# Optimization experiments

Measured on AMD Instinct MI355X. Metric: run time of the kernel, lower is better.

Reference implementation:

```python
import jax, jax.numpy as jnp
import numpy as np

OUT, IN = 4096, 4096
BITS = 4
B, S = 4, 2048


def setup_inputs() -> dict:
    key = jax.random.key(0)
    k1, k2, k3, k4, k5, k6 = jax.random.split(key, 6)
    x = jax.random.normal(k1, (B, S, IN), dtype=jnp.float32)
    indices = jax.random.randint(k2, (OUT, IN), 0, 2 ** BITS, dtype=jnp.int32)
    centroids = jax.random.normal(k3, (2 ** BITS,), dtype=jnp.float32)
    # Pi stands in for the seeded rotation matrix (orthogonality not required for math check)
    Pi = jax.random.normal(k4, (IN, IN), dtype=jnp.float32) / np.sqrt(IN)
    row_norms = jax.random.uniform(k5, (OUT,), dtype=jnp.float32) + 0.5
    bias = jax.random.normal(k6, (OUT,), dtype=jnp.float32)
    return {"x": x, "indices": indices, "centroids": centroids, "Pi": Pi,
            "row_norms": row_norms, "bias": bias}


def reference(x, indices, centroids, Pi, row_norms, bias):
    # Dequantize: centroid gather -> inverse rotation -> per-row rescale
    y_hat = centroids[indices]                    # (out, in)
    W = (y_hat @ Pi) * row_norms[:, None]         # (out, in)
    # F.linear: x @ W^T + b
    return jnp.einsum('bsi,oi->bso', x, W) + bias
```

## Files before the change

### kernel.cpp

```cpp
#include <hip/hip_runtime.h>
#include <hip/hip_bf16.h>

typedef unsigned short u16;
typedef __bf16 bf16x8 __attribute__((ext_vector_type(8)));
typedef float f32x16 __attribute__((ext_vector_type(16)));


__device__ __forceinline__ u16 f32_to_bf16(float f) {
    unsigned int u = __float_as_uint(f);
    unsigned int r = (u + 0x7FFFu + ((u >> 16) & 1u)) >> 16;
    return (u16)r;
}

__device__ __forceinline__ unsigned pack2(float a, float b) {
    return (unsigned)f32_to_bf16(a) | ((unsigned)f32_to_bf16(b) << 16);
}

__device__ __forceinline__ void load_lds16(const void* g, void* s) {
    __builtin_amdgcn_global_load_lds(
        (__attribute__((address_space(1))) void*)g,
        (__attribute__((address_space(3))) void*)s,
        16, 0, 0);
}


__global__ __launch_bounds__(256) void convert_f32_bf16(
        const float* __restrict__ in, u16* __restrict__ out) {
    int i = blockIdx.x * 256 + threadIdx.x;
    const float4* in4 = (const float4*)in;
    float4 v0 = in4[(size_t)i * 2];
    float4 v1 = in4[(size_t)i * 2 + 1];
    uint4 r;
    r.x = pack2(v0.x, v0.y);
    r.y = pack2(v0.z, v0.w);
    r.z = pack2(v1.x, v1.y);
    r.w = pack2(v1.z, v1.w);
    ((uint4*)out)[i] = r;
}


__global__ __launch_bounds__(256) void dequant_kernel(
        const int* __restrict__ idx, const float* __restrict__ cent,
        u16* __restrict__ out) {
    __shared__ float lut[16];
    if (threadIdx.x < 16) lut[threadIdx.x] = cent[threadIdx.x];
    __syncthreads();
    int i = blockIdx.x * 256 + threadIdx.x;
    const int4* in4 = (const int4*)idx;
    int4 a = in4[(size_t)i * 2];
    int4 b = in4[(size_t)i * 2 + 1];
    uint4 r;
    r.x = pack2(lut[a.x], lut[a.y]);
    r.y = pack2(lut[a.z], lut[a.w]);
    r.z = pack2(lut[b.x], lut[b.y]);
    r.w = pack2(lut[b.z], lut[b.w]);
    ((uint4*)out)[i] = r;
}


__global__ __launch_bounds__(256) void transpose_to_bf16(
        const float* __restrict__ Pi, u16* __restrict__ PiT) {
    __shared__ float tile[32][33];
    const int tx = threadIdx.x;
    const int ty = threadIdx.y;
    const int j0 = blockIdx.x * 32;
    const int k0 = blockIdx.y * 32;
#pragma unroll
    for (int i = 0; i < 4; i++)
        tile[ty + 8 * i][tx] = Pi[(size_t)(k0 + ty + 8 * i) * 4096 + j0 + tx];
    __syncthreads();
#pragma unroll
    for (int i = 0; i < 4; i++)
        PiT[(size_t)(j0 + ty + 8 * i) * 4096 + k0 + tx] =
            f32_to_bf16(tile[tx][ty + 8 * i]);
}


template <int MODE>
__global__ __launch_bounds__(256) void gemm_bt(
        const u16* __restrict__ A, const u16* __restrict__ Bm,
        const float* __restrict__ aux, float* __restrict__ Cf,
        u16* __restrict__ Cb, int M, int N, int K) {
    __shared__ u16 As[2 * 128 * 32];
    __shared__ u16 Bs[2 * 128 * 32];

    const int tid  = threadIdx.x;
    const int lane = tid & 63;
    const int wv   = tid >> 6;
    const int wr   = (wv >> 1) << 6;
    const int wc   = (wv & 1) << 6;
    const int m0   = blockIdx.y * 128;
    const int n0   = blockIdx.x * 128;

    const int rT  = tid >> 2;
    const int cSw = (((tid & 3) ^ ((rT >> 1) & 3)) << 3);
    const u16* Ag = A + (size_t)(m0 + rT) * K + cSw;
    const u16* Bg = Bm + (size_t)(n0 + rT) * K + cSw;
    u16* Asd = &As[tid * 8];
    u16* Bsd = &Bs[tid * 8];

    const int mrow = lane & 31;
    const int kc   = lane >> 5;
    int offA[2][2], offB[2][2];
#pragma unroll
    for (int mi = 0; mi < 2; mi++) {
        const int r  = wr + mi * 32 + mrow;
        const int sw = (r >> 1) & 3;
#pragma unroll
        for (int s = 0; s < 2; s++)
            offA[mi][s] = r * 32 + (((s * 2 + kc) ^ sw) << 3);
    }
#pragma unroll
    for (int ni = 0; ni < 2; ni++) {
        const int r  = wc + ni * 32 + mrow;
        const int sw = (r >> 1) & 3;
#pragma unroll
        for (int s = 0; s < 2; s++)
            offB[ni][s] = r * 32 + (((s * 2 + kc) ^ sw) << 3);
    }

    f32x16 acc[2][2];
#pragma unroll
    for (int i = 0; i < 2; i++)
#pragma unroll
        for (int j = 0; j < 2; j++)
#pragma unroll
            for (int e = 0; e < 16; e++) acc[i][j][e] = 0.f;

    for (int k0 = 0; k0 < K; k0 += 64) {
        load_lds16(Ag + k0, Asd);
        load_lds16(Ag + (size_t)64 * K + k0, Asd + 64 * 32);
        load_lds16(Bg + k0, Bsd);
        load_lds16(Bg + (size_t)64 * K + k0, Bsd + 64 * 32);
        load_lds16(Ag + k0 + 32, Asd + 4096);
        load_lds16(Ag + (size_t)64 * K + k0 + 32, Asd + 4096 + 64 * 32);
        load_lds16(Bg + k0 + 32, Bsd + 4096);
        load_lds16(Bg + (size_t)64 * K + k0 + 32, Bsd + 4096 + 64 * 32);
        __syncthreads();

#pragma unroll
        for (int h = 0; h < 2; h++) {
            const int hb = h * 4096;
            bf16x8 af[2][2], bfv[2][2];
#pragma unroll
            for (int mi = 0; mi < 2; mi++)
#pragma unroll
                for (int s = 0; s < 2; s++)
                    af[mi][s] = *(const bf16x8*)&As[hb + offA[mi][s]];
#pragma unroll
            for (int ni = 0; ni < 2; ni++)
#pragma unroll
                for (int s = 0; s < 2; s++)
                    bfv[ni][s] = *(const bf16x8*)&Bs[hb + offB[ni][s]];
#pragma unroll
            for (int s = 0; s < 2; s++)
#pragma unroll
                for (int mi = 0; mi < 2; mi++)
#pragma unroll
                    for (int ni = 0; ni < 2; ni++)
                        acc[mi][ni] = __builtin_amdgcn_mfma_f32_32x32x16_bf16(
                            af[mi][s], bfv[ni][s], acc[mi][ni], 0, 0, 0);
        }
        __syncthreads();
    }

    const int colf = lane & 31;
    const int r4   = (lane >> 5) << 2;
#pragma unroll
    for (int mi = 0; mi < 2; mi++) {
#pragma unroll
        for (int ni = 0; ni < 2; ni++) {
            const int col = n0 + wc + ni * 32 + colf;
            float bv = 0.f;
            if (MODE == 1) bv = aux[col];
#pragma unroll
            for (int reg = 0; reg < 16; reg++) {
                const int row = m0 + wr + mi * 32 + (reg & 3) + ((reg >> 2) << 3) + r4;
                if (MODE == 0)
                    Cb[(size_t)row * N + col] = f32_to_bf16(acc[mi][ni][reg] * aux[row]);
                else
                    Cf[(size_t)row * N + col] = acc[mi][ni][reg] + bv;
            }
        }
    }
}


extern "C" void kernel_launch(void* const* d_in, const int* in_sizes, int n_in,
                              void* d_out, int out_size, void* d_ws, size_t ws_size,
                              hipStream_t stream) {
    const float* x         = (const float*)d_in[0];
    const int*   indices   = (const int*)d_in[1];
    const float* centroids = (const float*)d_in[2];
    const float* Pi        = (const float*)d_in[3];
    const float* row_norms = (const float*)d_in[4];
    const float* bias      = (const float*)d_in[5];
    float* out = (float*)d_out;

    u16* x_bf = (u16*)d_ws;
    u16* y_bf = x_bf + (size_t)33554432;
    u16* pi_t = y_bf + (size_t)16777216;
    u16* w_bf = pi_t + (size_t)16777216;

    convert_f32_bf16<<<16384, 256, 0, stream>>>(x, x_bf);
    dequant_kernel<<<8192, 256, 0, stream>>>(indices, centroids, y_bf);
    transpose_to_bf16<<<dim3(128, 128), dim3(32, 8), 0, stream>>>(Pi, pi_t);
    gemm_bt<0><<<dim3(32, 32), 256, 0, stream>>>(
        y_bf, pi_t, row_norms, nullptr, w_bf, 4096, 4096, 4096);
    gemm_bt<1><<<dim3(32, 64), 256, 0, stream>>>(
        x_bf, w_bf, bias, out, nullptr, 8192, 4096, 4096);
}
```

Measured before the change: 774.1 us.

## Rewrite GEMM as 256x256-tile, 8-wave kernel with 4-stage LDS pipeline

Replaces the 128x128 double-buffered GEMM with a 256x256 tile computed by 512 threads (8 waves, each 128x64) using 16x16x32 MFMAs. A four-slot LDS ring is filled with direct global-to-LDS loads, and explicit vmcnt waits and barriers let loads overlap compute in half-step phases. It also remaps block IDs in groups of eight for L2 locality and raises wave priority around MFMA bursts. The larger tile cuts global traffic per FLOP but uses 128 KB of LDS and many accumulator registers, which limits occupancy and makes correctness depend on hand-tuned wait counts.

```diff
diff --git a/kernel.cpp b/kernel.cpp
--- a/kernel.cpp
+++ b/kernel.cpp
@@ -3,7 +3,7 @@
 
 typedef unsigned short u16;
 typedef __bf16 bf16x8 __attribute__((ext_vector_type(8)));
-typedef float f32x16 __attribute__((ext_vector_type(16)));
+typedef float f32x4 __attribute__((ext_vector_type(4)));
 
 
 __device__ __forceinline__ u16 f32_to_bf16(float f) {
@@ -77,109 +77,142 @@
 
 
 template <int MODE>
-__global__ __launch_bounds__(256) void gemm_bt(
+__global__ __launch_bounds__(512, 2) void gemm_bt(
         const u16* __restrict__ A, const u16* __restrict__ Bm,
         const float* __restrict__ aux, float* __restrict__ Cf,
         u16* __restrict__ Cb, int M, int N, int K) {
-    __shared__ u16 As[2 * 128 * 32];
-    __shared__ u16 Bs[2 * 128 * 32];
+    __shared__ u16 As[4 * 8192];
+    __shared__ u16 Bs[4 * 8192];
 
     const int tid  = threadIdx.x;
     const int lane = tid & 63;
     const int wv   = tid >> 6;
-    const int wr   = (wv >> 1) << 6;
-    const int wc   = (wv & 1) << 6;
-    const int m0   = blockIdx.y * 128;
-    const int n0   = blockIdx.x * 128;
-
-    const int rT  = tid >> 2;
-    const int cSw = (((tid & 3) ^ ((rT >> 1) & 3)) << 3);
-    const u16* Ag = A + (size_t)(m0 + rT) * K + cSw;
-    const u16* Bg = Bm + (size_t)(n0 + rT) * K + cSw;
-    u16* Asd = &As[tid * 8];
-    u16* Bsd = &Bs[tid * 8];
-
-    const int mrow = lane & 31;
-    const int kc   = lane >> 5;
-    int offA[2][2], offB[2][2];
-#pragma unroll
-    for (int mi = 0; mi < 2; mi++) {
-        const int r  = wr + mi * 32 + mrow;
-        const int sw = (r >> 1) & 3;
-#pragma unroll
-        for (int s = 0; s < 2; s++)
-            offA[mi][s] = r * 32 + (((s * 2 + kc) ^ sw) << 3);
-    }
-#pragma unroll
-    for (int ni = 0; ni < 2; ni++) {
-        const int r  = wc + ni * 32 + mrow;
-        const int sw = (r >> 1) & 3;
-#pragma unroll
-        for (int s = 0; s < 2; s++)
-            offB[ni][s] = r * 32 + (((s * 2 + kc) ^ sw) << 3);
-    }
-
-    f32x16 acc[2][2];
-#pragma unroll
-    for (int i = 0; i < 2; i++)
-#pragma unroll
-        for (int j = 0; j < 2; j++)
-#pragma unroll
-            for (int e = 0; e < 16; e++) acc[i][j][e] = 0.f;
-
-    for (int k0 = 0; k0 < K; k0 += 64) {
-        load_lds16(Ag + k0, Asd);
-        load_lds16(Ag + (size_t)64 * K + k0, Asd + 64 * 32);
-        load_lds16(Bg + k0, Bsd);
-        load_lds16(Bg + (size_t)64 * K + k0, Bsd + 64 * 32);
-        load_lds16(Ag + k0 + 32, Asd + 4096);
-        load_lds16(Ag + (size_t)64 * K + k0 + 32, Asd + 4096 + 64 * 32);
-        load_lds16(Bg + k0 + 32, Bsd + 4096);
-        load_lds16(Bg + (size_t)64 * K + k0 + 32, Bsd + 4096 + 64 * 32);
-        __syncthreads();
-
-#pragma unroll
-        for (int h = 0; h < 2; h++) {
-            const int hb = h * 4096;
-            bf16x8 af[2][2], bfv[2][2];
-#pragma unroll
-            for (int mi = 0; mi < 2; mi++)
-#pragma unroll
-                for (int s = 0; s < 2; s++)
-                    af[mi][s] = *(const bf16x8*)&As[hb + offA[mi][s]];
-#pragma unroll
-            for (int ni = 0; ni < 2; ni++)
-#pragma unroll
-                for (int s = 0; s < 2; s++)
-                    bfv[ni][s] = *(const bf16x8*)&Bs[hb + offB[ni][s]];
-#pragma unroll
-            for (int s = 0; s < 2; s++)
-#pragma unroll
-                for (int mi = 0; mi < 2; mi++)
-#pragma unroll
-                    for (int ni = 0; ni < 2; ni++)
-                        acc[mi][ni] = __builtin_amdgcn_mfma_f32_32x32x16_bf16(
-                            af[mi][s], bfv[ni][s], acc[mi][ni], 0, 0, 0);
-        }
-        __syncthreads();
-    }
-
-    const int colf = lane & 31;
-    const int r4   = (lane >> 5) << 2;
-#pragma unroll
-    for (int mi = 0; mi < 2; mi++) {
-#pragma unroll
-        for (int ni = 0; ni < 2; ni++) {
-            const int col = n0 + wc + ni * 32 + colf;
-            float bv = 0.f;
-            if (MODE == 1) bv = aux[col];
-#pragma unroll
-            for (int reg = 0; reg < 16; reg++) {
-                const int row = m0 + wr + mi * 32 + (reg & 3) + ((reg >> 2) << 3) + r4;
-                if (MODE == 0)
-                    Cb[(size_t)row * N + col] = f32_to_bf16(acc[mi][ni][reg] * aux[row]);
-                else
-                    Cf[(size_t)row * N + col] = acc[mi][ni][reg] + bv;
+    const int wr   = wv >> 2;
+    const int wc   = wv & 3;
+
+    const int nwg  = gridDim.x * gridDim.y;
+    const int orig = blockIdx.y * gridDim.x + blockIdx.x;
+    const int swz  = (orig & 7) * (nwg >> 3) + (orig >> 3);
+    const int m0   = (swz >> 4) << 8;
+    const int n0   = (swz & 15) << 8;
+
+    const int sr  = tid >> 2;
+    const int csw = ((tid & 3) ^ ((tid >> 3) & 3)) << 3;
+    const u16* a0 = A  + (size_t)(m0 + sr) * K + csw;
+    const u16* a1 = A  + (size_t)(m0 + 128 + sr) * K + csw;
+    const u16* b0 = Bm + (size_t)(n0 + sr) * K + csw;
+    const u16* b1 = Bm + (size_t)(n0 + 128 + sr) * K + csw;
+    u16* dA = As + tid * 8;
+    u16* dB = Bs + tid * 8;
+
+    const int l15   = lane & 15;
+    const int ck    = (((lane >> 4) ^ ((lane >> 1) & 3)) << 3);
+    const int laneA = (wr * 128 + l15) * 32 + ck;
+    const int laneB = (wc * 64 + l15) * 32 + ck;
+
+    f32x4 acc[8][4];
+#pragma unroll
+    for (int i = 0; i < 8; i++)
+#pragma unroll
+        for (int j = 0; j < 4; j++) acc[i][j] = (f32x4){0.f, 0.f, 0.f, 0.f};
+    bf16x8 bF[4];
+
+#define STAGE_A(SLOT, COL) do { \
+        load_lds16(a0 + (COL), dA + (SLOT) * 8192); \
+        load_lds16(a1 + (COL), dA + (SLOT) * 8192 + 4096); } while (0)
+#define STAGE_B(SLOT, COL) do { \
+        load_lds16(b0 + (COL), dB + (SLOT) * 8192); \
+        load_lds16(b1 + (COL), dB + (SLOT) * 8192 + 4096); } while (0)
+#define VM(N) asm volatile("s_waitcnt vmcnt(" #N ")" ::: "memory")
+
+#define PHASE(SB, MH, RB, STAGE, WAIT) do { \
+        bf16x8 aF[4]; \
+        _Pragma("unroll") \
+        for (int i_ = 0; i_ < 4; i_++) \
+            aF[i_] = *(const bf16x8*)&As[(SB) + laneA + ((MH) * 4 + i_) * 512]; \
+        if (RB) { \
+            _Pragma("unroll") \
+            for (int i_ = 0; i_ < 4; i_++) \
+                bF[i_] = *(const bf16x8*)&Bs[(SB) + laneB + i_ * 512]; \
+        } \
+        STAGE; \
+        WAIT; \
+        __builtin_amdgcn_s_barrier(); \
+        asm volatile("s_waitcnt lgkmcnt(0)" ::: "memory"); \
+        __builtin_amdgcn_sched_barrier(0); \
+        __builtin_amdgcn_s_setprio(1); \
+        _Pragma("unroll") \
+        for (int i_ = 0; i_ < 4; i_++) { \
+            _Pragma("unroll") \
+            for (int n_ = 0; n_ < 4; n_++) \
+                acc[(MH) * 4 + i_][n_] = __builtin_amdgcn_mfma_f32_16x16x32_bf16( \
+                    aF[i_], bF[n_], acc[(MH) * 4 + i_][n_], 0, 0, 0); \
+        } \
+        __builtin_amdgcn_s_setprio(0); \
+        __builtin_amdgcn_s_barrier(); \
+    } while (0)
+
+    const int NT = K >> 6;
+
+    STAGE_A(0, 0);
+    STAGE_B(0, 0);
+    STAGE_A(1, 32);
+    STAGE_B(1, 32);
+    STAGE_A(2, 64);
+    VM(6);
+    __builtin_amdgcn_s_barrier();
+
+#pragma unroll 1
+    for (int t = 0; t < NT - 2; t += 2) {
+        const int c1 = (t + 1) * 64;
+        const int c2 = c1 + 64;
+        PHASE(0,     0, 1, STAGE_B(2, c1),      ((void)0));
+        PHASE(0,     1, 0, STAGE_A(3, c1 + 32), VM(6));
+        PHASE(8192,  0, 1, STAGE_B(3, c1 + 32), ((void)0));
+        PHASE(8192,  1, 0, STAGE_A(0, c2),      VM(6));
+        PHASE(16384, 0, 1, STAGE_B(0, c2),      ((void)0));
+        PHASE(16384, 1, 0, STAGE_A(1, c2 + 32), VM(6));
+        PHASE(24576, 0, 1, STAGE_B(1, c2 + 32), ((void)0));
+        PHASE(24576, 1, 0, STAGE_A(2, c2 + 64), VM(6));
+    }
+
+    {
+        const int cT = (NT - 1) * 64;
+        PHASE(0,    0, 1, STAGE_B(2, cT),      ((void)0));
+        PHASE(0,    1, 0, STAGE_A(3, cT + 32), VM(6));
+        PHASE(8192, 0, 1, STAGE_B(3, cT + 32), ((void)0));
+        PHASE(8192, 1, 0, ((void)0),           VM(4));
+    }
+    {
+        PHASE(16384, 0, 1, ((void)0), ((void)0));
+        PHASE(16384, 1, 0, ((void)0), VM(0));
+        PHASE(24576, 0, 1, ((void)0), ((void)0));
+        PHASE(24576, 1, 0, ((void)0), ((void)0));
+    }
+
+#undef PHASE
+#undef VM
+#undef STAGE_B
+#undef STAGE_A
+
+    const int colf = l15;
+    const int r0   = (lane >> 4) << 2;
+#pragma unroll
+    for (int m = 0; m < 8; m++) {
+        const int row = m0 + wr * 128 + m * 16 + r0;
+#pragma unroll
+        for (int n = 0; n < 4; n++) {
+            const int col = n0 + wc * 64 + n * 16 + colf;
+            if (MODE == 0) {
+#pragma unroll
+                for (int e = 0; e < 4; e++)
+                    Cb[(size_t)(row + e) * N + col] =
+                        f32_to_bf16(acc[m][n][e] * aux[row + e]);
+            } else {
+                const float bv = aux[col];
+#pragma unroll
+                for (int e = 0; e < 4; e++)
+                    Cf[(size_t)(row + e) * N + col] = acc[m][n][e] + bv;
             }
         }
     }
@@ -205,8 +238,8 @@
     convert_f32_bf16<<<16384, 256, 0, stream>>>(x, x_bf);
     dequant_kernel<<<8192, 256, 0, stream>>>(indices, centroids, y_bf);
     transpose_to_bf16<<<dim3(128, 128), dim3(32, 8), 0, stream>>>(Pi, pi_t);
-    gemm_bt<0><<<dim3(32, 32), 256, 0, stream>>>(
+    gemm_bt<0><<<dim3(16, 16), 512, 0, stream>>>(
         y_bf, pi_t, row_norms, nullptr, w_bf, 4096, 4096, 4096);
-    gemm_bt<1><<<dim3(32, 64), 256, 0, stream>>>(
+    gemm_bt<1><<<dim3(16, 32), 512, 0, stream>>>(
         x_bf, w_bf, bias, out, nullptr, 8192, 4096, 4096);
 }
```

New measurement: 718.6 us. 7.2% less time.
